# Optimization experiments

Measured on AMD Instinct MI355X. Metric: run time of the kernel, lower is better.

The kernel has to match this reference:

```python
import jax, jax.numpy as jnp
import numpy as np

N_NODES = 100000
N_EDGES = 1600000
IN_FEATS = 256
OUT_FEATS = 128


def setup_inputs() -> dict:
    key = jax.random.key(0)
    k1, k2, k3, k4 = jax.random.split(key, 4)
    feat = jax.random.normal(k1, (N_NODES, IN_FEATS), dtype=jnp.float32)
    W = jax.random.normal(k2, (IN_FEATS, OUT_FEATS), dtype=jnp.float32)
    src = jax.random.randint(k3, (N_EDGES,), 0, N_NODES, dtype=jnp.int64)
    dst = jax.random.randint(k4, (N_EDGES,), 0, N_NODES, dtype=jnp.int64)
    return {"feat": feat, "W": W, "src": src, "dst": dst}


def reference(feat, W, src, dst):
    # h_self = feat @ W  -> [N, out_feats]
    h_self = feat @ W
    # update_all(copy_src('h','m'), sum('m','neigh')): gather source features,
    # scatter-sum at destination nodes (SpMM over the edge list).
    msgs = h_self[src]                                        # [E, out_feats]
    h_neigh = jax.ops.segment_sum(msgs, dst, num_segments=N_NODES)
    # in-degree per node
    degs = jax.ops.segment_sum(jnp.ones(dst.shape, jnp.float32), dst,
                               num_segments=N_NODES)          # [N]
    rst = (h_neigh + h_self) / (degs[:, None] + 1.0)
    return jax.nn.relu(rst)
```

## Files before the change

### kernel.cpp

```cpp
#include <hip/hip_runtime.h>
#include <hip/hip_bf16.h>


#define IN_FEATS 256
#define OUT_FEATS 128
#define NUM_NODES 100000
#define NUM_EDGES 1600000

#define NB 782
#define EC 128
#define CHUNK_E 12500
#define BCAP 3072
#define GEMM_BLOCKS 782

typedef __attribute__((ext_vector_type(8))) short short8;
typedef __attribute__((ext_vector_type(8))) unsigned short ushort8;
typedef __attribute__((ext_vector_type(4))) float f32x4;

static __device__ inline unsigned short f2bfu(float x) {
    union { __hip_bfloat16 h; unsigned short u; } c;
    c.h = __float2bfloat16(x);
    return c.u;
}
static __device__ inline ushort2 f2bfu2(float x, float y) {
    union { __hip_bfloat162 h; ushort2 u; } c;
    c.h = __float22bfloat162_rn(make_float2(x, y));
    return c.u;
}
static __device__ inline float bf2f(unsigned short h) {
    return __uint_as_float((unsigned)h << 16);
}

__global__ __launch_bounds__(256) void convert_hist(
    const float* __restrict__ W, unsigned short* __restrict__ Wt,
    const int* __restrict__ dst, int* __restrict__ counts)
{
    int b = blockIdx.x;
    int t = threadIdx.x;
    if (b < 128) {
        int i = b * 256 + t;
        int n = i >> 8;
        int k = i & 255;
        Wt[i] = f2bfu(W[(size_t)k * OUT_FEATS + n]);
        return;
    }
    int c = b - 128;
    __shared__ int hist[NB];
    for (int i = t; i < NB; i += 256) hist[i] = 0;
    __syncthreads();
    const int4* dp = (const int4*)(dst + c * CHUNK_E);
    for (int i = t; i < CHUNK_E / 4; i += 256) {
        int4 d4 = dp[i];
        atomicAdd(&hist[d4.x >> 7], 1);
        atomicAdd(&hist[d4.y >> 7], 1);
        atomicAdd(&hist[d4.z >> 7], 1);
        atomicAdd(&hist[d4.w >> 7], 1);
    }
    __syncthreads();
    for (int i = t; i < NB; i += 256) counts[c * NB + i] = hist[i];
}

__global__ __launch_bounds__(128) void scan_chunks(
    int* __restrict__ counts, int* __restrict__ bucket_total)
{
    __shared__ int sd[128];
    int b = blockIdx.x, t = threadIdx.x;
    int v = counts[t * NB + b];
    sd[t] = v;
    __syncthreads();
    for (int o = 1; o < 128; o <<= 1) {
        int x = (t >= o) ? sd[t - o] : 0;
        __syncthreads();
        sd[t] += x;
        __syncthreads();
    }
    counts[t * NB + b] = sd[t] - v;
    if (t == 127) bucket_total[b] = sd[127];
}

__global__ __launch_bounds__(256) void scan_buckets(
    const int* __restrict__ bucket_total, int* __restrict__ bucket_base)
{
    __shared__ int sd[256];
    int t = threadIdx.x;
    int base = t * 4;
    int v0 = 0, v1 = 0, v2 = 0, v3 = 0;
    if (base + 3 < NB) {
        int4 v = *(const int4*)&bucket_total[base];
        v0 = v.x; v1 = v.y; v2 = v.z; v3 = v.w;
    } else {
        if (base + 0 < NB) v0 = bucket_total[base + 0];
        if (base + 1 < NB) v1 = bucket_total[base + 1];
        if (base + 2 < NB) v2 = bucket_total[base + 2];
        if (base + 3 < NB) v3 = bucket_total[base + 3];
    }
    int s = v0 + v1 + v2 + v3;
    sd[t] = s;
    __syncthreads();
    for (int o = 1; o < 256; o <<= 1) {
        int x = (t >= o) ? sd[t - o] : 0;
        __syncthreads();
        sd[t] += x;
        __syncthreads();
    }
    int e0 = sd[t] - s, e1 = e0 + v0, e2 = e1 + v1, e3 = e2 + v2;
    if (base + 0 < NB) bucket_base[base + 0] = e0;
    if (base + 1 < NB) bucket_base[base + 1] = e1;
    if (base + 2 < NB) bucket_base[base + 2] = e2;
    if (base + 3 < NB) bucket_base[base + 3] = e3;
}

__global__ __launch_bounds__(512) void scatter_k(
    const int* __restrict__ src, const int* __restrict__ dst,
    const int* __restrict__ counts, const int* __restrict__ bucket_base,
    int* __restrict__ bedges)
{
    __shared__ int cur[NB];
    const int tid = threadIdx.x;
    int c = blockIdx.x;
    for (int i = tid; i < NB; i += 512)
        cur[i] = bucket_base[i] + counts[c * NB + i];
    __syncthreads();
    const int4* dp = (const int4*)(dst + c * CHUNK_E);
    const int4* sp = (const int4*)(src + c * CHUNK_E);
    for (int i = tid; i < CHUNK_E / 4; i += 512) {
        int4 d4 = dp[i];
        int4 s4 = sp[i];
        int dv[4] = { d4.x, d4.y, d4.z, d4.w };
        int sv[4] = { s4.x, s4.y, s4.z, s4.w };
#pragma unroll
        for (int j = 0; j < 4; ++j) {
            int d = dv[j];
            int slot = atomicAdd(&cur[d >> 7], 1);
            bedges[slot] = sv[j] | ((d & 127) << 17);
        }
    }
}

static __device__ __forceinline__ void stage_chunk(
    const float* __restrict__ feat, char* smem, int buf,
    int bm0, int k0, int t, int M)
{
#pragma unroll
    for (int j = 0; j < 4; ++j) {
        int G = j * 256 + t;
        int r = G >> 3;
        int g = G & 7;
        int srow = bm0 + r;
        if (srow > M - 1) srow = M - 1;
        const float* src = feat + (size_t)srow * IN_FEATS + k0 + ((g ^ (r & 7)) << 2);
        __builtin_amdgcn_global_load_lds(
            (const __attribute__((address_space(1))) unsigned int*)src,
            (__attribute__((address_space(3))) unsigned int*)(smem + buf * 16384 + G * 16),
            16, 0, 0);
    }
}

template<int KC>
static __device__ __forceinline__ void gemm_step(
    const float* __restrict__ feat, const unsigned short* __restrict__ Wt,
    char* smem_raw, f32x4 (&acc)[2][8], short8 (&bf)[8],
    int w32, int lf, int lg, int bm0, int tid, int M)
{
    asm volatile("s_waitcnt vmcnt(%0)" :: "n"((KC == 7) ? 8 : 12) : "memory");
    __builtin_amdgcn_s_barrier();
    __builtin_amdgcn_sched_barrier(0);

    short8 af[2];
#pragma unroll
    for (int mt = 0; mt < 2; ++mt) {
        int r  = w32 + mt * 16 + lf;
        int rs = r & 7;
        const char* base = smem_raw + (KC % 3) * 16384 + r * 128;
        float4 f0 = *(const float4*)(base + ((((lg << 1) + 0) ^ rs) << 4));
        float4 f1 = *(const float4*)(base + ((((lg << 1) + 1) ^ rs) << 4));
        ushort2 c0 = f2bfu2(f0.x, f0.y);
        ushort2 c1 = f2bfu2(f0.z, f0.w);
        ushort2 c2 = f2bfu2(f1.x, f1.y);
        ushort2 c3 = f2bfu2(f1.z, f1.w);
        af[mt] = (short8){ (short)c0.x, (short)c0.y, (short)c1.x, (short)c1.y,
                           (short)c2.x, (short)c2.y, (short)c3.x, (short)c3.y };
    }

#pragma unroll
    for (int q = 0; q < 8; ++q) {
        acc[0][q] = __builtin_amdgcn_mfma_f32_16x16x32_bf16(af[0], bf[q], acc[0][q], 0, 0, 0);
        acc[1][q] = __builtin_amdgcn_mfma_f32_16x16x32_bf16(af[1], bf[q], acc[1][q], 0, 0, 0);
    }

    if (KC < 7) {
#pragma unroll
        for (int q = 0; q < 8; ++q)
            bf[q] = *(const short8*)(Wt + (size_t)(q * 16 + lf) * IN_FEATS
                                        + ((KC + 1) * 4 + lg) * 8);
    }
    if (KC < 6)
        stage_chunk(feat, smem_raw, (KC + 2) % 3, bm0, (KC + 2) * 32, tid, M);
}

__global__ __launch_bounds__(256, 2) void gemm_k(
    const float* __restrict__ feat, const unsigned short* __restrict__ Wt,
    unsigned short* __restrict__ hself16, int M)
{
    __shared__ char smem_raw[49152];
    const int tid = threadIdx.x;
    const int w   = tid >> 6;
    const int l   = tid & 63;
    const int lf  = l & 15;
    const int lg  = (l >> 4) & 3;
    const int w32 = w * 32;
    const int bm0 = blockIdx.x * 128;

    f32x4 acc[2][8];
#pragma unroll
    for (int mt = 0; mt < 2; ++mt)
#pragma unroll
        for (int nt = 0; nt < 8; ++nt)
            acc[mt][nt] = (f32x4){0.f, 0.f, 0.f, 0.f};

    short8 bf[8];
    stage_chunk(feat, smem_raw, 0, bm0, 0, tid, M);
    asm volatile("" ::: "memory");
#pragma unroll
    for (int q = 0; q < 8; ++q)
        bf[q] = *(const short8*)(Wt + (size_t)(q * 16 + lf) * IN_FEATS + lg * 8);
    asm volatile("" ::: "memory");
    stage_chunk(feat, smem_raw, 1, bm0, 32, tid, M);

    gemm_step<0>(feat, Wt, smem_raw, acc, bf, w32, lf, lg, bm0, tid, M);
    gemm_step<1>(feat, Wt, smem_raw, acc, bf, w32, lf, lg, bm0, tid, M);
    gemm_step<2>(feat, Wt, smem_raw, acc, bf, w32, lf, lg, bm0, tid, M);
    gemm_step<3>(feat, Wt, smem_raw, acc, bf, w32, lf, lg, bm0, tid, M);
    gemm_step<4>(feat, Wt, smem_raw, acc, bf, w32, lf, lg, bm0, tid, M);
    gemm_step<5>(feat, Wt, smem_raw, acc, bf, w32, lf, lg, bm0, tid, M);
    gemm_step<6>(feat, Wt, smem_raw, acc, bf, w32, lf, lg, bm0, tid, M);
    gemm_step<7>(feat, Wt, smem_raw, acc, bf, w32, lf, lg, bm0, tid, M);

    __syncthreads();
    unsigned short* ep = (unsigned short*)smem_raw;
#pragma unroll
    for (int mt = 0; mt < 2; ++mt)
#pragma unroll
        for (int nt = 0; nt < 8; ++nt)
#pragma unroll
            for (int r = 0; r < 4; ++r) {
                int row = w32 + mt * 16 + lg * 4 + r;
                ep[row * 128 + nt * 16 + lf] = f2bfu(acc[mt][nt][r]);
            }
    __syncthreads();
#pragma unroll
    for (int i = 0; i < 8; ++i) {
        int lrow = w32 + i * 4 + (l >> 4);
        ushort8 v = *(const ushort8*)(ep + lrow * 128 + (l & 15) * 8);
        int grow = bm0 + lrow;
        if (grow < M)
            *(ushort8*)(hself16 + (size_t)grow * OUT_FEATS + (l & 15) * 8) = v;
    }
}

__global__ __launch_bounds__(512, 4) void sort_gather(
    const int* __restrict__ bucket_base, const int* __restrict__ bucket_total,
    const int* __restrict__ bedges, const unsigned short* __restrict__ hself16,
    float* __restrict__ out)
{
    __shared__ int sorted[BCAP];
    __shared__ int cnt[128], off[128], cursor[128], sd[128];

    int b = blockIdx.x, t = threadIdx.x;
    int base = bucket_base[b];
    int tot = bucket_total[b];
    if (tot > BCAP) tot = BCAP;
    int nnodes = NUM_NODES - b * 128;
    if (nnodes > 128) nnodes = 128;

    if (t < 128) cnt[t] = 0;
    __syncthreads();
    for (int i = t; i < tot; i += 512)
        atomicAdd(&cnt[bedges[base + i] >> 17], 1);
    __syncthreads();
    if (t < 128) sd[t] = cnt[t];
    __syncthreads();
    for (int o = 1; o < 128; o <<= 1) {
        int x = 0;
        if (t < 128 && t >= o) x = sd[t - o];
        __syncthreads();
        if (t < 128) sd[t] += x;
        __syncthreads();
    }
    if (t < 128) { int e = sd[t] - cnt[t]; off[t] = e; cursor[t] = e; }
    __syncthreads();
    for (int i = t; i < tot; i += 512) {
        int e = bedges[base + i];
        int r = atomicAdd(&cursor[e >> 17], 1);
        sorted[r] = e & 0x1FFFF;
    }
    __syncthreads();

    const int gid = t >> 4;
    const int lf  = t & 15;

#pragma unroll
    for (int rep = 0; rep < 4; ++rep) {
        int ln = rep * 32 + gid;
        if (ln >= nnodes) continue;
        int beg = off[ln];
        int cn  = cnt[ln];
        int end = beg + cn;
        int n = b * 128 + ln;
        ushort8 hs = *(const ushort8*)(hself16 + (size_t)n * OUT_FEATS + lf * 8);

        float acc[8];
#pragma unroll
        for (int i = 0; i < 8; ++i) acc[i] = 0.f;

        for (int j0 = beg; j0 < end; j0 += 8) {
            int  ss[8];
            bool pp[8];
#pragma unroll
            for (int q = 0; q < 8; ++q) {
                int jj = j0 + q;
                pp[q] = jj < end;
                ss[q] = pp[q] ? sorted[jj] : 0;
            }
            ushort8 h[8];
#pragma unroll
            for (int q = 0; q < 8; ++q)
                h[q] = *(const ushort8*)(hself16 + (size_t)ss[q] * OUT_FEATS + lf * 8);
#pragma unroll
            for (int q = 0; q < 8; ++q)
                if (pp[q]) {
#pragma unroll
                    for (int i = 0; i < 8; ++i) acc[i] += bf2f(h[q][i]);
                }
        }

        float inv = 1.0f / (float)(cn + 1);
        float v[8];
#pragma unroll
        for (int i = 0; i < 8; ++i)
            v[i] = fmaxf((acc[i] + bf2f(hs[i])) * inv, 0.f);
        float4* op = (float4*)(out + (size_t)n * OUT_FEATS + lf * 8);
        op[0] = make_float4(v[0], v[1], v[2], v[3]);
        op[1] = make_float4(v[4], v[5], v[6], v[7]);
    }
}

extern "C" void kernel_launch(void* const* d_in, const int* in_sizes, int n_in,
                              void* d_out, int out_size, void* d_ws, size_t ws_size,
                              hipStream_t stream) {
    const float* feat = (const float*)d_in[0];
    const float* W    = (const float*)d_in[1];
    const int*   src  = (const int*)d_in[2];
    const int*   dst  = (const int*)d_in[3];
    float* out = (float*)d_out;

    char* ws = (char*)d_ws;
    unsigned short* hself16 = (unsigned short*)ws;
    unsigned short* Wt      = (unsigned short*)(ws + 25600000);
    int* counts       = (int*)(ws + 25665536);
    int* bucket_total = (int*)(ws + 26065920);
    int* bucket_base  = (int*)(ws + 26069120);
    int* bedges       = (int*)(ws + 26072320);

    convert_hist<<<256, 256, 0, stream>>>(W, Wt, dst, counts);
    scan_chunks<<<NB, 128, 0, stream>>>(counts, bucket_total);
    scan_buckets<<<1, 256, 0, stream>>>(bucket_total, bucket_base);
    scatter_k<<<EC, 512, 0, stream>>>(src, dst, counts, bucket_base, bedges);
    gemm_k<<<GEMM_BLOCKS, 256, 0, stream>>>(feat, Wt, hself16, NUM_NODES);
    sort_gather<<<NB, 512, 0, stream>>>(bucket_base, bucket_total, bedges,
                                        hself16, out);
}
```

Baseline: 293.0 us.

## Co-schedule GEMM tiles with edge-bucketing stages in fused launches

The separate histogram, scan and scatter kernels and the standalone GEMM are merged into one multi-role kernel launched four times. Each launch runs one edge-preprocessing stage plus a slice of GEMM row tiles (150+100+42+490 = 782), so the tensor-core GEMM overlaps the latency-bound sorting stages. The cost is that the edge stages now run with 256 threads and 48KB LDS at the GEMM's occupancy limits, and the split of GEMM tiles across launches is hand-tuned.

```diff
diff --git a/kernel.cpp b/kernel.cpp
--- a/kernel.cpp
+++ b/kernel.cpp
@@ -13,6 +13,16 @@
 #define BCAP 3072
 #define GEMM_BLOCKS 782
 
+#define GA 150
+#define GB 100
+#define GC 42
+#define GD 490
+
+#define ST_HIST  0
+#define ST_SCANC 1
+#define ST_SCANB 2
+#define ST_SCAT  3
+
 typedef __attribute__((ext_vector_type(8))) short short8;
 typedef __attribute__((ext_vector_type(8))) unsigned short ushort8;
 typedef __attribute__((ext_vector_type(4))) float f32x4;
@@ -31,110 +41,13 @@
     return __uint_as_float((unsigned)h << 16);
 }
 
-__global__ __launch_bounds__(256) void convert_hist(
-    const float* __restrict__ W, unsigned short* __restrict__ Wt,
-    const int* __restrict__ dst, int* __restrict__ counts)
-{
-    int b = blockIdx.x;
-    int t = threadIdx.x;
-    if (b < 128) {
-        int i = b * 256 + t;
-        int n = i >> 8;
-        int k = i & 255;
-        Wt[i] = f2bfu(W[(size_t)k * OUT_FEATS + n]);
-        return;
-    }
-    int c = b - 128;
-    __shared__ int hist[NB];
-    for (int i = t; i < NB; i += 256) hist[i] = 0;
-    __syncthreads();
-    const int4* dp = (const int4*)(dst + c * CHUNK_E);
-    for (int i = t; i < CHUNK_E / 4; i += 256) {
-        int4 d4 = dp[i];
-        atomicAdd(&hist[d4.x >> 7], 1);
-        atomicAdd(&hist[d4.y >> 7], 1);
-        atomicAdd(&hist[d4.z >> 7], 1);
-        atomicAdd(&hist[d4.w >> 7], 1);
-    }
-    __syncthreads();
-    for (int i = t; i < NB; i += 256) counts[c * NB + i] = hist[i];
-}
-
-__global__ __launch_bounds__(128) void scan_chunks(
-    int* __restrict__ counts, int* __restrict__ bucket_total)
-{
-    __shared__ int sd[128];
-    int b = blockIdx.x, t = threadIdx.x;
-    int v = counts[t * NB + b];
-    sd[t] = v;
-    __syncthreads();
-    for (int o = 1; o < 128; o <<= 1) {
-        int x = (t >= o) ? sd[t - o] : 0;
-        __syncthreads();
-        sd[t] += x;
-        __syncthreads();
-    }
-    counts[t * NB + b] = sd[t] - v;
-    if (t == 127) bucket_total[b] = sd[127];
-}
-
-__global__ __launch_bounds__(256) void scan_buckets(
-    const int* __restrict__ bucket_total, int* __restrict__ bucket_base)
-{
-    __shared__ int sd[256];
-    int t = threadIdx.x;
-    int base = t * 4;
-    int v0 = 0, v1 = 0, v2 = 0, v3 = 0;
-    if (base + 3 < NB) {
-        int4 v = *(const int4*)&bucket_total[base];
-        v0 = v.x; v1 = v.y; v2 = v.z; v3 = v.w;
-    } else {
-        if (base + 0 < NB) v0 = bucket_total[base + 0];
-        if (base + 1 < NB) v1 = bucket_total[base + 1];
-        if (base + 2 < NB) v2 = bucket_total[base + 2];
-        if (base + 3 < NB) v3 = bucket_total[base + 3];
-    }
-    int s = v0 + v1 + v2 + v3;
-    sd[t] = s;
-    __syncthreads();
-    for (int o = 1; o < 256; o <<= 1) {
-        int x = (t >= o) ? sd[t - o] : 0;
-        __syncthreads();
-        sd[t] += x;
-        __syncthreads();
-    }
-    int e0 = sd[t] - s, e1 = e0 + v0, e2 = e1 + v1, e3 = e2 + v2;
-    if (base + 0 < NB) bucket_base[base + 0] = e0;
-    if (base + 1 < NB) bucket_base[base + 1] = e1;
-    if (base + 2 < NB) bucket_base[base + 2] = e2;
-    if (base + 3 < NB) bucket_base[base + 3] = e3;
-}
-
-__global__ __launch_bounds__(512) void scatter_k(
-    const int* __restrict__ src, const int* __restrict__ dst,
-    const int* __restrict__ counts, const int* __restrict__ bucket_base,
-    int* __restrict__ bedges)
-{
-    __shared__ int cur[NB];
-    const int tid = threadIdx.x;
-    int c = blockIdx.x;
-    for (int i = tid; i < NB; i += 512)
-        cur[i] = bucket_base[i] + counts[c * NB + i];
-    __syncthreads();
-    const int4* dp = (const int4*)(dst + c * CHUNK_E);
-    const int4* sp = (const int4*)(src + c * CHUNK_E);
-    for (int i = tid; i < CHUNK_E / 4; i += 512) {
-        int4 d4 = dp[i];
-        int4 s4 = sp[i];
-        int dv[4] = { d4.x, d4.y, d4.z, d4.w };
-        int sv[4] = { s4.x, s4.y, s4.z, s4.w };
-#pragma unroll
-        for (int j = 0; j < 4; ++j) {
-            int d = dv[j];
-            int slot = atomicAdd(&cur[d >> 7], 1);
-            bedges[slot] = sv[j] | ((d & 127) << 17);
-        }
-    }
+__global__ __launch_bounds__(256) void convert_wt(
+    const float* __restrict__ W, unsigned short* __restrict__ Wt)
+{
+    int i = blockIdx.x * 256 + threadIdx.x;
+    int n = i >> 8;
+    int k = i & 255;
+    Wt[i] = f2bfu(W[(size_t)k * OUT_FEATS + n]);
 }
 
 static __device__ __forceinline__ void stage_chunk(
@@ -198,18 +111,17 @@
         stage_chunk(feat, smem_raw, (KC + 2) % 3, bm0, (KC + 2) * 32, tid, M);
 }
 
-__global__ __launch_bounds__(256, 2) void gemm_k(
+static __device__ __forceinline__ void gemm_body(
     const float* __restrict__ feat, const unsigned short* __restrict__ Wt,
-    unsigned short* __restrict__ hself16, int M)
-{
-    __shared__ char smem_raw[49152];
+    unsigned short* __restrict__ hself16, int M, int gb, char* smem_raw)
+{
     const int tid = threadIdx.x;
     const int w   = tid >> 6;
     const int l   = tid & 63;
     const int lf  = l & 15;
     const int lg  = (l >> 4) & 3;
     const int w32 = w * 32;
-    const int bm0 = blockIdx.x * 128;
+    const int bm0 = gb * 128;
 
     f32x4 acc[2][8];
 #pragma unroll
@@ -258,6 +170,105 @@
     }
 }
 
+__global__ __launch_bounds__(256, 2) void fused_k(
+    int stage, int nedge, int gemm_base,
+    const float* __restrict__ feat, const unsigned short* __restrict__ Wt,
+    unsigned short* __restrict__ hself16, int M,
+    const int* __restrict__ src, const int* __restrict__ dst,
+    int* __restrict__ counts, int* __restrict__ bucket_total,
+    int* __restrict__ bucket_base, int* __restrict__ bedges)
+{
+    __shared__ char smem_raw[49152];
+    const int t = threadIdx.x;
+
+    if ((int)blockIdx.x < nedge) {
+        int b = blockIdx.x;
+        if (stage == ST_HIST) {
+            int* hist = (int*)smem_raw;
+            int c = b;
+            for (int i = t; i < NB; i += 256) hist[i] = 0;
+            __syncthreads();
+            const int4* dp = (const int4*)(dst + c * CHUNK_E);
+            for (int i = t; i < CHUNK_E / 4; i += 256) {
+                int4 d4 = dp[i];
+                atomicAdd(&hist[d4.x >> 7], 1);
+                atomicAdd(&hist[d4.y >> 7], 1);
+                atomicAdd(&hist[d4.z >> 7], 1);
+                atomicAdd(&hist[d4.w >> 7], 1);
+            }
+            __syncthreads();
+            for (int i = t; i < NB; i += 256) counts[c * NB + i] = hist[i];
+        } else if (stage == ST_SCANC) {
+            int* sd = (int*)smem_raw;
+            int v = 0;
+            if (t < 128) { v = counts[t * NB + b]; sd[t] = v; }
+            __syncthreads();
+            for (int o = 1; o < 128; o <<= 1) {
+                int x = 0;
+                if (t < 128 && t >= o) x = sd[t - o];
+                __syncthreads();
+                if (t < 128) sd[t] += x;
+                __syncthreads();
+            }
+            if (t < 128) {
+                counts[t * NB + b] = sd[t] - v;
+                if (t == 127) bucket_total[b] = sd[127];
+            }
+        } else if (stage == ST_SCANB) {
+            int* sd = (int*)smem_raw;
+            int base = t * 4;
+            int v0 = 0, v1 = 0, v2 = 0, v3 = 0;
+            if (base + 3 < NB) {
+                int4 v = *(const int4*)&bucket_total[base];
+                v0 = v.x; v1 = v.y; v2 = v.z; v3 = v.w;
+            } else {
+                if (base + 0 < NB) v0 = bucket_total[base + 0];
+                if (base + 1 < NB) v1 = bucket_total[base + 1];
+                if (base + 2 < NB) v2 = bucket_total[base + 2];
+                if (base + 3 < NB) v3 = bucket_total[base + 3];
+            }
+            int s = v0 + v1 + v2 + v3;
+            sd[t] = s;
+            __syncthreads();
+            for (int o = 1; o < 256; o <<= 1) {
+                int x = (t >= o) ? sd[t - o] : 0;
+                __syncthreads();
+                sd[t] += x;
+                __syncthreads();
+            }
+            int e0 = sd[t] - s, e1 = e0 + v0, e2 = e1 + v1, e3 = e2 + v2;
+            if (base + 0 < NB) bucket_base[base + 0] = e0;
+            if (base + 1 < NB) bucket_base[base + 1] = e1;
+            if (base + 2 < NB) bucket_base[base + 2] = e2;
+            if (base + 3 < NB) bucket_base[base + 3] = e3;
+        } else {
+            int* cur = (int*)smem_raw;
+            int c = b;
+            for (int i = t; i < NB; i += 256)
+                cur[i] = bucket_base[i] + counts[c * NB + i];
+            __syncthreads();
+            const int4* dp = (const int4*)(dst + c * CHUNK_E);
+            const int4* sp = (const int4*)(src + c * CHUNK_E);
+            for (int i = t; i < CHUNK_E / 4; i += 256) {
+                int4 d4 = dp[i];
+                int4 s4 = sp[i];
+                int dv[4] = { d4.x, d4.y, d4.z, d4.w };
+                int sv[4] = { s4.x, s4.y, s4.z, s4.w };
+#pragma unroll
+                for (int j = 0; j < 4; ++j) {
+                    int d = dv[j];
+                    int slot = atomicAdd(&cur[d >> 7], 1);
+                    bedges[slot] = sv[j] | ((d & 127) << 17);
+                }
+            }
+        }
+        return;
+    }
+
+    int gb = gemm_base + (int)blockIdx.x - nedge;
+    gemm_body(feat, Wt, hself16, M, gb, smem_raw);
+}
+
 __global__ __launch_bounds__(512, 4) void sort_gather(
     const int* __restrict__ bucket_base, const int* __restrict__ bucket_total,
     const int* __restrict__ bedges, const unsigned short* __restrict__ hself16,
@@ -362,11 +373,15 @@
     int* bucket_base  = (int*)(ws + 26069120);
     int* bedges       = (int*)(ws + 26072320);
 
-    convert_hist<<<256, 256, 0, stream>>>(W, Wt, dst, counts);
-    scan_chunks<<<NB, 128, 0, stream>>>(counts, bucket_total);
-    scan_buckets<<<1, 256, 0, stream>>>(bucket_total, bucket_base);
-    scatter_k<<<EC, 512, 0, stream>>>(src, dst, counts, bucket_base, bedges);
-    gemm_k<<<GEMM_BLOCKS, 256, 0, stream>>>(feat, Wt, hself16, NUM_NODES);
+    convert_wt<<<128, 256, 0, stream>>>(W, Wt);
+    fused_k<<<EC + GA, 256, 0, stream>>>(ST_HIST, EC, 0,
+        feat, Wt, hself16, NUM_NODES, src, dst, counts, bucket_total, bucket_base, bedges);
+    fused_k<<<NB + GB, 256, 0, stream>>>(ST_SCANC, NB, GA,
+        feat, Wt, hself16, NUM_NODES, src, dst, counts, bucket_total, bucket_base, bedges);
+    fused_k<<<1 + GC, 256, 0, stream>>>(ST_SCANB, 1, GA + GB,
+        feat, Wt, hself16, NUM_NODES, src, dst, counts, bucket_total, bucket_base, bedges);
+    fused_k<<<EC + GD, 256, 0, stream>>>(ST_SCAT, EC, GA + GB + GC,
+        feat, Wt, hself16, NUM_NODES, src, dst, counts, bucket_total, bucket_base, bedges);
     sort_gather<<<NB, 512, 0, stream>>>(bucket_base, bucket_total, bedges,
                                         hself16, out);
 }
```

Measured after the change: 311.6 us. 1.06x slower.

## Fuse edge bucketing into GEMM kernel using fixed-capacity buckets and global atomics

Applied to the files above, without the earlier changes.

Replaces the histogram/two-scan/scatter pipeline with fixed-capacity per-bucket regions (BCAP slots each), where chunk offsets come from global atomicAdd on per-bucket counters instead of prefix scans. The bucketing blocks are merged into the GEMM launch as extra blocks, so edge scattering runs concurrently with the matmul and three kernel launches disappear. The trade-off is that edges beyond BCAP per bucket are silently dropped, and edge order within a bucket becomes nondeterministic.

```diff
diff --git a/kernel.cpp b/kernel.cpp
--- a/kernel.cpp
+++ b/kernel.cpp
@@ -31,9 +31,9 @@
     return __uint_as_float((unsigned)h << 16);
 }
 
-__global__ __launch_bounds__(256) void convert_hist(
+__global__ __launch_bounds__(256) void setup_k(
     const float* __restrict__ W, unsigned short* __restrict__ Wt,
-    const int* __restrict__ dst, int* __restrict__ counts)
+    int* __restrict__ gcnt)
 {
     int b = blockIdx.x;
     int t = threadIdx.x;
@@ -44,97 +44,7 @@
         Wt[i] = f2bfu(W[(size_t)k * OUT_FEATS + n]);
         return;
     }
-    int c = b - 128;
-    __shared__ int hist[NB];
-    for (int i = t; i < NB; i += 256) hist[i] = 0;
-    __syncthreads();
-    const int4* dp = (const int4*)(dst + c * CHUNK_E);
-    for (int i = t; i < CHUNK_E / 4; i += 256) {
-        int4 d4 = dp[i];
-        atomicAdd(&hist[d4.x >> 7], 1);
-        atomicAdd(&hist[d4.y >> 7], 1);
-        atomicAdd(&hist[d4.z >> 7], 1);
-        atomicAdd(&hist[d4.w >> 7], 1);
-    }
-    __syncthreads();
-    for (int i = t; i < NB; i += 256) counts[c * NB + i] = hist[i];
-}
-
-__global__ __launch_bounds__(128) void scan_chunks(
-    int* __restrict__ counts, int* __restrict__ bucket_total)
-{
-    __shared__ int sd[128];
-    int b = blockIdx.x, t = threadIdx.x;
-    int v = counts[t * NB + b];
-    sd[t] = v;
-    __syncthreads();
-    for (int o = 1; o < 128; o <<= 1) {
-        int x = (t >= o) ? sd[t - o] : 0;
-        __syncthreads();
-        sd[t] += x;
-        __syncthreads();
-    }
-    counts[t * NB + b] = sd[t] - v;
-    if (t == 127) bucket_total[b] = sd[127];
-}
-
-__global__ __launch_bounds__(256) void scan_buckets(
-    const int* __restrict__ bucket_total, int* __restrict__ bucket_base)
-{
-    __shared__ int sd[256];
-    int t = threadIdx.x;
-    int base = t * 4;
-    int v0 = 0, v1 = 0, v2 = 0, v3 = 0;
-    if (base + 3 < NB) {
-        int4 v = *(const int4*)&bucket_total[base];
-        v0 = v.x; v1 = v.y; v2 = v.z; v3 = v.w;
-    } else {
-        if (base + 0 < NB) v0 = bucket_total[base + 0];
-        if (base + 1 < NB) v1 = bucket_total[base + 1];
-        if (base + 2 < NB) v2 = bucket_total[base + 2];
-        if (base + 3 < NB) v3 = bucket_total[base + 3];
-    }
-    int s = v0 + v1 + v2 + v3;
-    sd[t] = s;
-    __syncthreads();
-    for (int o = 1; o < 256; o <<= 1) {
-        int x = (t >= o) ? sd[t - o] : 0;
-        __syncthreads();
-        sd[t] += x;
-        __syncthreads();
-    }
-    int e0 = sd[t] - s, e1 = e0 + v0, e2 = e1 + v1, e3 = e2 + v2;
-    if (base + 0 < NB) bucket_base[base + 0] = e0;
-    if (base + 1 < NB) bucket_base[base + 1] = e1;
-    if (base + 2 < NB) bucket_base[base + 2] = e2;
-    if (base + 3 < NB) bucket_base[base + 3] = e3;
-}
-
-__global__ __launch_bounds__(512) void scatter_k(
-    const int* __restrict__ src, const int* __restrict__ dst,
-    const int* __restrict__ counts, const int* __restrict__ bucket_base,
-    int* __restrict__ bedges)
-{
-    __shared__ int cur[NB];
-    const int tid = threadIdx.x;
-    int c = blockIdx.x;
-    for (int i = tid; i < NB; i += 512)
-        cur[i] = bucket_base[i] + counts[c * NB + i];
-    __syncthreads();
-    const int4* dp = (const int4*)(dst + c * CHUNK_E);
-    const int4* sp = (const int4*)(src + c * CHUNK_E);
-    for (int i = tid; i < CHUNK_E / 4; i += 512) {
-        int4 d4 = dp[i];
-        int4 s4 = sp[i];
-        int dv[4] = { d4.x, d4.y, d4.z, d4.w };
-        int sv[4] = { s4.x, s4.y, s4.z, s4.w };
-#pragma unroll
-        for (int j = 0; j < 4; ++j) {
-            int d = dv[j];
-            int slot = atomicAdd(&cur[d >> 7], 1);
-            bedges[slot] = sv[j] | ((d & 127) << 17);
-        }
-    }
+    for (int i = t; i < NB; i += 256) gcnt[i] = 0;
 }
 
 static __device__ __forceinline__ void stage_chunk(
@@ -198,18 +108,17 @@
         stage_chunk(feat, smem_raw, (KC + 2) % 3, bm0, (KC + 2) * 32, tid, M);
 }
 
-__global__ __launch_bounds__(256, 2) void gemm_k(
+static __device__ __forceinline__ void gemm_body(
     const float* __restrict__ feat, const unsigned short* __restrict__ Wt,
-    unsigned short* __restrict__ hself16, int M)
-{
-    __shared__ char smem_raw[49152];
+    unsigned short* __restrict__ hself16, int M, int gb, char* smem_raw)
+{
     const int tid = threadIdx.x;
     const int w   = tid >> 6;
     const int l   = tid & 63;
     const int lf  = l & 15;
     const int lg  = (l >> 4) & 3;
     const int w32 = w * 32;
-    const int bm0 = blockIdx.x * 128;
+    const int bm0 = gb * 128;
 
     f32x4 acc[2][8];
 #pragma unroll
@@ -258,17 +167,66 @@
     }
 }
 
+__global__ __launch_bounds__(256, 2) void gemm_scatter(
+    const float* __restrict__ feat, const unsigned short* __restrict__ Wt,
+    unsigned short* __restrict__ hself16, int M,
+    const int* __restrict__ src, const int* __restrict__ dst,
+    int* __restrict__ gcnt, int* __restrict__ bedges)
+{
+    __shared__ char smem_raw[49152];
+    const int t = threadIdx.x;
+
+    if ((int)blockIdx.x < EC) {
+        int c = blockIdx.x;
+        int* hist = (int*)smem_raw;
+        int* cur  = hist + NB;
+        for (int i = t; i < NB; i += 256) hist[i] = 0;
+        __syncthreads();
+        const int4* dp = (const int4*)(dst + c * CHUNK_E);
+        const int4* sp = (const int4*)(src + c * CHUNK_E);
+        for (int i = t; i < CHUNK_E / 4; i += 256) {
+            int4 d4 = dp[i];
+            atomicAdd(&hist[d4.x >> 7], 1);
+            atomicAdd(&hist[d4.y >> 7], 1);
+            atomicAdd(&hist[d4.z >> 7], 1);
+            atomicAdd(&hist[d4.w >> 7], 1);
+        }
+        __syncthreads();
+        for (int i = t; i < NB; i += 256) {
+            int h = hist[i];
+            cur[i] = h ? atomicAdd(&gcnt[i], h) : 0;
+        }
+        __syncthreads();
+        for (int i = t; i < CHUNK_E / 4; i += 256) {
+            int4 d4 = dp[i];
+            int4 s4 = sp[i];
+            int dv[4] = { d4.x, d4.y, d4.z, d4.w };
+            int sv[4] = { s4.x, s4.y, s4.z, s4.w };
+#pragma unroll
+            for (int j = 0; j < 4; ++j) {
+                int d = dv[j];
+                int b = d >> 7;
+                int slot = atomicAdd(&cur[b], 1);
+                if (slot < BCAP)
+                    bedges[b * BCAP + slot] = sv[j] | ((d & 127) << 17);
+            }
+        }
+        return;
+    }
+
+    gemm_body(feat, Wt, hself16, M, (int)blockIdx.x - EC, smem_raw);
+}
+
 __global__ __launch_bounds__(512, 4) void sort_gather(
-    const int* __restrict__ bucket_base, const int* __restrict__ bucket_total,
-    const int* __restrict__ bedges, const unsigned short* __restrict__ hself16,
-    float* __restrict__ out)
+    const int* __restrict__ gcnt, const int* __restrict__ bedges,
+    const unsigned short* __restrict__ hself16, float* __restrict__ out)
 {
     __shared__ int sorted[BCAP];
     __shared__ int cnt[128], off[128], cursor[128], sd[128];
 
     int b = blockIdx.x, t = threadIdx.x;
-    int base = bucket_base[b];
-    int tot = bucket_total[b];
+    int base = b * BCAP;
+    int tot = gcnt[b];
     if (tot > BCAP) tot = BCAP;
     int nnodes = NUM_NODES - b * 128;
     if (nnodes > 128) nnodes = 128;
@@ -357,16 +315,11 @@
     char* ws = (char*)d_ws;
     unsigned short* hself16 = (unsigned short*)ws;
     unsigned short* Wt      = (unsigned short*)(ws + 25600000);
-    int* counts       = (int*)(ws + 25665536);
-    int* bucket_total = (int*)(ws + 26065920);
-    int* bucket_base  = (int*)(ws + 26069120);
-    int* bedges       = (int*)(ws + 26072320);
-
-    convert_hist<<<256, 256, 0, stream>>>(W, Wt, dst, counts);
-    scan_chunks<<<NB, 128, 0, stream>>>(counts, bucket_total);
-    scan_buckets<<<1, 256, 0, stream>>>(bucket_total, bucket_base);
-    scatter_k<<<EC, 512, 0, stream>>>(src, dst, counts, bucket_base, bedges);
-    gemm_k<<<GEMM_BLOCKS, 256, 0, stream>>>(feat, Wt, hself16, NUM_NODES);
-    sort_gather<<<NB, 512, 0, stream>>>(bucket_base, bucket_total, bedges,
-                                        hself16, out);
-}
+    int* gcnt         = (int*)(ws + 25665536);
+    int* bedges       = (int*)(ws + 25668736);
+
+    setup_k<<<129, 256, 0, stream>>>(W, Wt, gcnt);
+    gemm_scatter<<<EC + GEMM_BLOCKS, 256, 0, stream>>>(
+        feat, Wt, hself16, NUM_NODES, src, dst, gcnt, bedges);
+    sort_gather<<<NB, 512, 0, stream>>>(gcnt, bedges, hself16, out);
+}
```

Result: faster. 279.3 us (-4.7%).
